# Optimization experiments

Hardware: AMD Instinct MI355X
Metric: run time of the kernel (lower is better)

The kernel has to match this reference:

```python
import jax, jax.numpy as jnp
import numpy as np

B, L, E, D, H, P, NL = 4, 2048, 7, 512, 8, 720, 2
DH = D // H
FACTOR = 5
U = min(L, FACTOR * int(np.ceil(np.log(L))))  # top-u queries, = 40
SCALE = 1.0 / np.sqrt(DH)


def setup_inputs() -> dict:
    key = jax.random.key(0)
    ks = jax.random.split(key, 12)
    s = 0.02
    rn = lambda k, shape: jax.random.normal(k, shape, jnp.float32) * s
    return {
        "x": jax.random.normal(ks[0], (B, L, E), jnp.float32),
        "emb_w": rn(ks[1], (E, D)), "emb_b": jnp.zeros((D,), jnp.float32),
        "Wq": rn(ks[2], (NL, D, D)), "bq": jnp.zeros((NL, D), jnp.float32),
        "Wk": rn(ks[3], (NL, D, D)), "bk": jnp.zeros((NL, D), jnp.float32),
        "Wv": rn(ks[4], (NL, D, D)), "bv": jnp.zeros((NL, D), jnp.float32),
        "Wo": rn(ks[5], (NL, D, D)), "bo": jnp.zeros((NL, D), jnp.float32),
        "W1": rn(ks[6], (NL, D, D)), "b1": jnp.zeros((NL, D), jnp.float32),
        "W2": rn(ks[7], (NL, D, D)), "b2": jnp.zeros((NL, D), jnp.float32),
        "ln1_g": jnp.ones((NL, D), jnp.float32), "ln1_b": jnp.zeros((NL, D), jnp.float32),
        "ln2_g": jnp.ones((NL, D), jnp.float32), "ln2_b": jnp.zeros((NL, D), jnp.float32),
        "proj_w": rn(ks[8], (D, E)), "proj_b": jnp.zeros((E,), jnp.float32),
    }


def layer_norm(x, g, b):
    m = jnp.mean(x, axis=-1, keepdims=True)
    v = jnp.mean(jnp.square(x - m), axis=-1, keepdims=True)
    return (x - m) * jax.lax.rsqrt(v + 1e-5) * g + b


def prob_sparse_attn(x, Wq, bq, Wk, bk, Wv, bv, Wo, bo):
    # x: [B, L, D] -> heads [B, H, L, DH]
    q = (x @ Wq + bq).reshape(B, L, H, DH).transpose(0, 2, 1, 3)
    k = (x @ Wk + bk).reshape(B, L, H, DH).transpose(0, 2, 1, 3)
    v = (x @ Wv + bv).reshape(B, L, H, DH).transpose(0, 2, 1, 3)
    scores = jnp.einsum('bhqd,bhkd->bhqk', q, k) * SCALE  # [B,H,L,L]
    # sparsity measure M(q) = max_k - mean_k
    M = jnp.max(scores, axis=-1) - jnp.mean(scores, axis=-1)  # [B,H,L]
    _, idx = jax.lax.top_k(M, U)  # [B,H,U] indices of active queries
    s_top = jnp.take_along_axis(scores, idx[..., None], axis=2)  # [B,H,U,L]
    attn = jax.nn.softmax(s_top, axis=-1)
    upd = jnp.einsum('bhul,bhld->bhud', attn, v)  # [B,H,U,DH]
    # lazy queries get the mean of V; active queries get attention output
    ctx = jnp.broadcast_to(jnp.mean(v, axis=2, keepdims=True), v.shape)
    bidx = jnp.arange(B)[:, None, None]
    hidx = jnp.arange(H)[None, :, None]
    ctx = ctx.at[bidx, hidx, idx].set(upd)  # scatter active queries
    out = ctx.transpose(0, 2, 1, 3).reshape(B, L, D)
    return out @ Wo + bo


def reference(x, emb_w, emb_b, Wq, bq, Wk, bk, Wv, bv, Wo, bo,
              W1, b1, W2, b2, ln1_g, ln1_b, ln2_g, ln2_b, proj_w, proj_b):
    h = x @ emb_w + emb_b  # [B,L,D]
    for i in range(NL):
        a = prob_sparse_attn(h, Wq[i], bq[i], Wk[i], bk[i], Wv[i], bv[i], Wo[i], bo[i])
        h = layer_norm(h + a, ln1_g[i], ln1_b[i])
        f = jax.nn.relu(h @ W1[i] + b1[i]) @ W2[i] + b2[i]
        h = layer_norm(h + f, ln2_g[i], ln2_b[i])
    return h[:, -P:, :] @ proj_w + proj_b  # [B,P,E]
```

## Files before the change

kernel.cpp:

```cpp
#include <hip/hip_runtime.h>
#include <hip/hip_bf16.h>
#include <cstdint>
#include <cstddef>

#define BB 4
#define LL 2048
#define EE 7
#define DD 512
#define HH 8
#define DHH 64
#define PP 720
#define NLAYER 2
#define UU 40
#define SCALE 0.125f
#define ROWS (BB*LL)
#define BIGN ((size_t)ROWS*DD)
#define NIN 21
#define FCH 256
#define NCH (LL/FCH)
#define PSTR 264
#define VSTR 136

typedef unsigned short u16;
typedef unsigned long long u64;
typedef __bf16 bf16x8 __attribute__((ext_vector_type(8)));
typedef float  f32x4  __attribute__((ext_vector_type(4)));

__device__ __forceinline__ float bf2f(u16 u){
  union { uint32_t i; float f; } c; c.i = ((uint32_t)u) << 16; return c.f;
}
__device__ __forceinline__ u16 f2b(float f){
  __hip_bfloat16 h = __float2bfloat16(f);
  return *(u16*)&h;
}
__device__ __forceinline__ void gld_lds16(const u16* g, u16* l){
  __builtin_amdgcn_global_load_lds(
      (const __attribute__((address_space(1))) uint32_t*)g,
      (__attribute__((address_space(3))) uint32_t*)l, 16, 0, 0);
}
__device__ __forceinline__ int is_bf16(const void* d15){
  return (*(const uint32_t*)d15 == 0x3F800000u) ? 0 : 1;
}

#define NSMALL 15
struct ConvArgs { const void* src[NSMALL]; int off[NSMALL]; int n[NSMALL]; };
struct WPtrs { const void* p[6]; };

__global__ __launch_bounds__(256) void k_preamble(ConvArgs a, WPtrs wp,
    const void* __restrict__ xraw, const void* __restrict__ d15,
    float* __restrict__ dst, float* __restrict__ zbuf,
    u16* __restrict__ hB, u16* __restrict__ wT){
  int y = blockIdx.y, bx = blockIdx.x, t = threadIdx.x;
  int isbf = is_bf16(d15);
  __shared__ u16 tile[64][65];
  __shared__ float xs[32][EE];
  if (y < NSMALL){
    int i = bx*256 + t;
    if (i >= a.n[y]) return;
    float v;
    if (isbf) v = bf2f(((const u16*)a.src[y])[i]);
    else      v = ((const float*)a.src[y])[i];
    dst[(size_t)a.off[y] + i] = v;
  } else if (y == NSMALL){
    int i = bx*256 + t;
    if (i < NLAYER*4096) zbuf[i] = 0.f;
  } else if (y < 32){
    int flat = (y - 16)*256 + bx;
    if (flat >= 512) return;
    int colgrp = flat & 1;
    int rowbase = (flat >> 1) * 32;
    int dd = colgrp*256 + t;
    if (t < 32*EE){
      int j = t / EE, e = t - j*EE;
      xs[j][e] = isbf ? bf2f(((const u16*)xraw)[(rowbase + j)*EE + e])
                      : ((const float*)xraw)[(rowbase + j)*EE + e];
    }
    float wreg[EE];
    #pragma unroll
    for (int e=0;e<EE;e++)
      wreg[e] = isbf ? bf2f(((const u16*)a.src[1])[e*DD + dd])
                     : ((const float*)a.src[1])[e*DD + dd];
    float bias = isbf ? bf2f(((const u16*)a.src[2])[dd]) : ((const float*)a.src[2])[dd];
    __syncthreads();
    for (int j=0;j<32;j++){
      float acc = bias;
      #pragma unroll
      for (int e=0;e<EE;e++) acc = fmaf(xs[j][e], wreg[e], acc);
      hB[(size_t)(rowbase + j)*DD + dd] = f2b(acc);
    }
  } else {
    int flat = (y - 32)*256 + bx;
    int mz = flat >> 6, tl = flat & 63;
    int lay = mz / 6, mat = mz % 6;
    int n0 = (tl & 7)*64, k0 = (tl >> 3)*64;
    int r = t >> 6, c = t & 63;
    const void* src = wp.p[mat];
    for (int rr = r; rr < 64; rr += 4){
      size_t idx = ((size_t)lay*DD + (k0+rr))*DD + n0 + c;
      u16 v;
      if (isbf) v = ((const u16*)src)[idx];
      else      v = f2b(((const float*)src)[idx]);
      tile[rr][c] = v;
    }
    __syncthreads();
    u16* drow = wT + ((size_t)mz*DD + n0)*DD + k0;
    int c4 = (t & 15)*4;
    for (int rr = (t >> 4); rr < 64; rr += 16){
      ushort4 v = { tile[c4][rr], tile[c4+1][rr], tile[c4+2][rr], tile[c4+3][rr] };
      *(ushort4*)(drow + (size_t)rr*DD + c4) = v;
    }
  }
}

__global__ __launch_bounds__(256) void k_gemm_mfma(const u16* __restrict__ A, const u16* __restrict__ Bt,
    const float* __restrict__ bias, u16* __restrict__ Cb, int relu){
  __shared__ u16 As[64*64];
  __shared__ u16 Bs[128*64];
  int t = threadIdx.x, wave = t >> 6, lane = t & 63;
  int qlane = lane & 15, quad = lane >> 4;
  int flat = blockIdx.x + gridDim.x*blockIdx.y;
  int xcd = flat & 7, rest = flat >> 3;
  int mb = (xcd + 8*(rest & 15)) * 64;
  int nb = (rest >> 4) * 128;
  int wm = (wave & 1) * 32, wn = (wave >> 1) * 64;
  f32x4 acc[2][4];
  #pragma unroll
  for (int i=0;i<2;i++)
    #pragma unroll
    for (int j=0;j<4;j++) acc[i][j] = (f32x4){0.f,0.f,0.f,0.f};

  int srow = wave*8 + (lane>>3);
  int scol = (((lane&7) ^ ((lane>>3)&7))) * 8;
  const u16* Ag = A + (size_t)(mb + srow)*DD + scol;
  const u16* Bg = Bt + (size_t)(nb + srow)*DD + scol;

  for (int k0 = 0; k0 < DD; k0 += 64){
    __syncthreads();
    #pragma unroll
    for (int i=0;i<2;i++)
      gld_lds16(Ag + (size_t)i*32*DD + k0, As + (i*32 + wave*8)*64);
    #pragma unroll
    for (int i=0;i<4;i++)
      gld_lds16(Bg + (size_t)i*32*DD + k0, Bs + (i*32 + wave*8)*64);
    __syncthreads();
    #pragma unroll
    for (int ch=0; ch<2; ++ch){
      bf16x8 af[2], bfv[4];
      int cgL = ((ch*4 + quad) ^ (qlane & 7)) * 8;
      #pragma unroll
      for (int i=0;i<2;i++) af[i] = *(const bf16x8*)(As + (wm + i*16 + qlane)*64 + cgL);
      #pragma unroll
      for (int j=0;j<4;j++) bfv[j] = *(const bf16x8*)(Bs + (wn + j*16 + qlane)*64 + cgL);
      #pragma unroll
      for (int i=0;i<2;i++)
        #pragma unroll
        for (int j=0;j<4;j++)
          acc[i][j] = __builtin_amdgcn_mfma_f32_16x16x32_bf16(af[i], bfv[j], acc[i][j], 0, 0, 0);
    }
  }
  #pragma unroll
  for (int i=0;i<2;i++){
    int rbase = mb + wm + i*16 + quad*4;
    #pragma unroll
    for (int j=0;j<4;j++){
      int col = nb + wn + j*16 + qlane;
      float bv = bias[col];
      #pragma unroll
      for (int r=0;r<4;r++){
        float cv = acc[i][j][r] + bv;
        if (relu) cv = fmaxf(cv, 0.f);
        Cb[(size_t)(rbase + r)*DD + col] = f2b(cv);
      }
    }
  }
}

__global__ __launch_bounds__(256) void k_gemm_wo(const u64* __restrict__ rowPtr, const u16* __restrict__ Bt,
    const float* __restrict__ bias, u16* __restrict__ Cb){
  __shared__ u16 As[64*64];
  __shared__ u16 Bs[128*64];
  int t = threadIdx.x, wave = t >> 6, lane = t & 63;
  int qlane = lane & 15, quad = lane >> 4;
  int flat = blockIdx.x + gridDim.x*blockIdx.y;
  int xcd = flat & 7, rest = flat >> 3;
  int mb = (xcd + 8*(rest & 15)) * 64;
  int nb = (rest >> 4) * 128;
  int wm = (wave & 1) * 32, wn = (wave >> 1) * 64;
  f32x4 acc[2][4];
  #pragma unroll
  for (int i=0;i<2;i++)
    #pragma unroll
    for (int j=0;j<4;j++) acc[i][j] = (f32x4){0.f,0.f,0.f,0.f};

  int srow = wave*8 + (lane>>3);
  int scol = (((lane&7) ^ ((lane>>3)&7))) * 8;
  const u16* Bg = Bt + (size_t)(nb + srow)*DD + scol;

  for (int k0 = 0; k0 < DD; k0 += 64){
    int slice = k0 >> 6;
    __syncthreads();
    #pragma unroll
    for (int i=0;i<2;i++){
      int arow = mb + i*32 + srow;
      const u16* src = (const u16*)(uintptr_t)rowPtr[(size_t)arow*8 + slice] + scol;
      gld_lds16(src, As + (i*32 + wave*8)*64);
    }
    #pragma unroll
    for (int i=0;i<4;i++)
      gld_lds16(Bg + (size_t)i*32*DD + k0, Bs + (i*32 + wave*8)*64);
    __syncthreads();
    #pragma unroll
    for (int ch=0; ch<2; ++ch){
      bf16x8 af[2], bfv[4];
      int cgL = ((ch*4 + quad) ^ (qlane & 7)) * 8;
      #pragma unroll
      for (int i=0;i<2;i++) af[i] = *(const bf16x8*)(As + (wm + i*16 + qlane)*64 + cgL);
      #pragma unroll
      for (int j=0;j<4;j++) bfv[j] = *(const bf16x8*)(Bs + (wn + j*16 + qlane)*64 + cgL);
      #pragma unroll
      for (int i=0;i<2;i++)
        #pragma unroll
        for (int j=0;j<4;j++)
          acc[i][j] = __builtin_amdgcn_mfma_f32_16x16x32_bf16(af[i], bfv[j], acc[i][j], 0, 0, 0);
    }
  }
  #pragma unroll
  for (int i=0;i<2;i++){
    int rbase = mb + wm + i*16 + quad*4;
    #pragma unroll
    for (int j=0;j<4;j++){
      int col = nb + wn + j*16 + qlane;
      float bv = bias[col];
      #pragma unroll
      for (int r=0;r<4;r++){
        float cv = acc[i][j][r] + bv;
        Cb[(size_t)(rbase + r)*DD + col] = f2b(cv);
      }
    }
  }
}

__global__ __launch_bounds__(256) void k_gemm_qkv(const u16* __restrict__ A, const u16* __restrict__ Wt,
    const float* __restrict__ bq, const float* __restrict__ bk, const float* __restrict__ bv,
    u16* __restrict__ qB, u16* __restrict__ kB, u16* __restrict__ vB,
    float* __restrict__ ksum, float* __restrict__ vsum){
  __shared__ u16 As[128*64];
  __shared__ u16 Bs[128*64];
  int t = threadIdx.x, wave = t >> 6, lane = t & 63;
  int qlane = lane & 15, quad = lane >> 4;
  int flat = blockIdx.x + gridDim.x*blockIdx.y;
  int xcd = flat & 7, rest = flat >> 3;
  int mb  = (xcd + 8*(rest & 7)) * 128;
  int nbg = (rest >> 3) * 128;
  int sel = nbg >> 9;
  int nb  = nbg & 511;
  const float* bias = (sel==0) ? bq : (sel==1) ? bk : bv;
  u16* out = (sel==0) ? qB : (sel==1) ? kB : vB;
  const u16* Bt = Wt + (size_t)sel*DD*DD;
  int wm = (wave & 1) * 64, wn = (wave >> 1) * 64;
  f32x4 acc[4][4];
  #pragma unroll
  for (int i=0;i<4;i++)
    #pragma unroll
    for (int j=0;j<4;j++) acc[i][j] = (f32x4){0.f,0.f,0.f,0.f};

  int srow = wave*8 + (lane>>3);
  int scol = (((lane&7) ^ ((lane>>3)&7))) * 8;
  const u16* Ag = A + (size_t)(mb + srow)*DD + scol;
  const u16* Bg = Bt + (size_t)(nb + srow)*DD + scol;

  for (int k0 = 0; k0 < DD; k0 += 64){
    __syncthreads();
    #pragma unroll
    for (int i=0;i<4;i++){
      gld_lds16(Ag + (size_t)i*32*DD + k0, As + (i*32 + wave*8)*64);
      gld_lds16(Bg + (size_t)i*32*DD + k0, Bs + (i*32 + wave*8)*64);
    }
    __syncthreads();
    #pragma unroll
    for (int ch=0; ch<2; ++ch){
      bf16x8 af[4], bf[4];
      int cgL = ((ch*4 + quad) ^ (qlane & 7)) * 8;
      #pragma unroll
      for (int i=0;i<4;i++) af[i] = *(const bf16x8*)(As + (wm + i*16 + qlane)*64 + cgL);
      #pragma unroll
      for (int j=0;j<4;j++) bf[j] = *(const bf16x8*)(Bs + (wn + j*16 + qlane)*64 + cgL);
      #pragma unroll
      for (int i=0;i<4;i++)
        #pragma unroll
        for (int j=0;j<4;j++)
          acc[i][j] = __builtin_amdgcn_mfma_f32_16x16x32_bf16(af[i], bf[j], acc[i][j], 0, 0, 0);
    }
  }
  float csum[4] = {0.f,0.f,0.f,0.f};
  #pragma unroll
  for (int j=0;j<4;j++){
    int col = nb + wn + j*16 + qlane;
    float bvv = bias[col];
    #pragma unroll
    for (int i=0;i<4;i++){
      int rbase = mb + wm + i*16 + quad*4;
      #pragma unroll
      for (int r=0;r<4;r++){
        float cv = acc[i][j][r] + bvv;
        out[(size_t)(rbase + r)*DD + col] = f2b(cv);
        csum[j] += cv;
      }
    }
  }
  if (sel > 0){
    float* dst = (sel==1) ? ksum : vsum;
    int bidx = mb >> 11;
    #pragma unroll
    for (int j=0;j<4;j++){
      float v = csum[j];
      v += __shfl_xor(v, 16);
      v += __shfl_xor(v, 32);
      if ((lane>>4) == 0)
        atomicAdd(dst + bidx*512 + nb + wn + j*16 + lane, v);
    }
  }
}

__global__ __launch_bounds__(256) void k_sparsity_mfma(const u16* __restrict__ qB, const u16* __restrict__ kB,
    const float* __restrict__ ksum, float* __restrict__ Mout){
  int flat = blockIdx.x + gridDim.x*blockIdx.y;
  int xcd = flat & 7, rest = flat >> 3;
  int qc = rest & 15;
  int bh = (rest >> 4)*8 + xcd;
  int b = bh >> 3, hh = bh & 7;
  int q0 = qc * 128;
  int t = threadIdx.x, wave = t >> 6, lane = t & 63;
  const u16* qbase = qB + ((size_t)(b*LL + q0))*DD + hh*DHH;
  const u16* kbase = kB + ((size_t)b*LL)*DD + hh*DHH;
  bf16x8 qa[8][2];
  #pragma unroll
  for (int i=0;i<8;i++)
    #pragma unroll
    for (int c=0;c<2;c++)
      qa[i][c] = *(const bf16x8*)(qbase + (size_t)(i*16 + (lane&15))*DD + c*32 + (lane>>4)*8);
  float rmax[8][4];
  #pragma unroll
  for (int i=0;i<8;i++)
    #pragma unroll
    for (int r=0;r<4;r++) rmax[i][r] = -3.0e38f;
  for (int kt = wave*16; kt < LL; kt += 64){
    bf16x8 kb0 = *(const bf16x8*)(kbase + (size_t)(kt + (lane&15))*DD + (lane>>4)*8);
    bf16x8 kb1 = *(const bf16x8*)(kbase + (size_t)(kt + (lane&15))*DD + 32 + (lane>>4)*8);
    #pragma unroll
    for (int i=0;i<8;i++){
      f32x4 a = (f32x4){0.f,0.f,0.f,0.f};
      a = __builtin_amdgcn_mfma_f32_16x16x32_bf16(qa[i][0], kb0, a, 0, 0, 0);
      a = __builtin_amdgcn_mfma_f32_16x16x32_bf16(qa[i][1], kb1, a, 0, 0, 0);
      #pragma unroll
      for (int r=0;r<4;r++) rmax[i][r] = fmaxf(rmax[i][r], a[r]);
    }
  }
  #pragma unroll
  for (int i=0;i<8;i++)
    #pragma unroll
    for (int r=0;r<4;r++){
      float v = rmax[i][r];
      v = fmaxf(v, __shfl_xor(v, 1));
      v = fmaxf(v, __shfl_xor(v, 2));
      v = fmaxf(v, __shfl_xor(v, 4));
      v = fmaxf(v, __shfl_xor(v, 8));
      rmax[i][r] = v;
    }
  __shared__ float smax[4][128];
  if ((lane & 15) == 0){
    #pragma unroll
    for (int i=0;i<8;i++)
      #pragma unroll
      for (int r=0;r<4;r++)
        smax[wave][i*16 + (lane>>4)*4 + r] = rmax[i][r];
  }
  __syncthreads();
  if (t < 128){
    float mx = fmaxf(fmaxf(smax[0][t], smax[1][t]), fmaxf(smax[2][t], smax[3][t]));
    const u16* qrow = qB + (size_t)(b*LL + q0 + t)*DD + hh*DHH;
    float dot = 0.f;
    #pragma unroll
    for (int dv=0; dv<16; ++dv){
      ushort4 qv = *(const ushort4*)(qrow + dv*4);
      const float* kp = ksum + bh*DHH + dv*4;
      dot += bf2f(qv.x)*kp[0] + bf2f(qv.y)*kp[1]
           + bf2f(qv.z)*kp[2] + bf2f(qv.w)*kp[3];
    }
    Mout[bh*LL + q0 + t] = SCALE * (mx - dot * (1.0f/LL));
  }
}

__global__ __launch_bounds__(256) void k_flash(const u16* __restrict__ qB, const u16* __restrict__ kB,
    const u16* __restrict__ vB, const float* __restrict__ Mv, int* __restrict__ sidx,
    float* __restrict__ pO, float* __restrict__ pM, float* __restrict__ pS){
  int bh = blockIdx.y, c = blockIdx.x;
  int b = bh >> 3, hh = bh & 7;
  int t = threadIdx.x, w = t >> 6, lane = t & 63;
  int qlane = lane & 15, quad = lane >> 4;
  int l0 = c * FCH;
  __shared__ u16 Ps[48*PSTR];
  __shared__ union { uint32_t keys[LL]; u16 vst[64*VSTR]; } uu;
  __shared__ float wred[4][48];
  __shared__ float mrow[48];
  __shared__ int hist[256];
  __shared__ int scr[2];
  __shared__ int tieIdx[64];
  __shared__ int counters[2];
  __shared__ int sidxL[UU], sidxS[UU];

  {
    const float* src = Mv + (size_t)bh*LL;
    #pragma unroll
    for (int j = 0; j < 8; ++j){
      int idx = t + j*256;
      uint32_t u = __float_as_uint(src[idx]);
      uu.keys[idx] = (u & 0x80000000u) ? ~u : (u | 0x80000000u);
    }
    uint32_t prefix = 0, pmask = 0;
    int need = UU;
    #pragma unroll
    for (int pass = 0; pass < 4; ++pass){
      int shift = 24 - pass*8;
      __syncthreads();
      hist[t] = 0;
      __syncthreads();
      #pragma unroll
      for (int j = 0; j < 8; ++j){
        uint32_t k = uu.keys[t + j*256];
        if ((k & pmask) == prefix)
          atomicAdd(&hist[(k >> shift) & 0xFF], 1);
      }
      __syncthreads();
      if (t < 64){
        int ln = t;
        int h0 = hist[ln*4+0], h1 = hist[ln*4+1], h2 = hist[ln*4+2], h3 = hist[ln*4+3];
        int s = h0 + h1 + h2 + h3;
        int acc = s;
        #pragma unroll
        for (int off = 1; off < 64; off <<= 1){
          int v = __shfl_down(acc, off);
          if (ln + off < 64) acc += v;
        }
        int c3 = acc - s;
        int c2 = c3 + h3;
        int c1 = c2 + h2;
        int c0 = c1 + h1;
        if      (need > c3 && need <= c3 + h3){ scr[0] = ln*4+3; scr[1] = c3; }
        else if (need > c2 && need <= c2 + h2){ scr[0] = ln*4+2; scr[1] = c2; }
        else if (need > c1 && need <= c1 + h1){ scr[0] = ln*4+1; scr[1] = c1; }
        else if (need > c0 && need <= c0 + h0){ scr[0] = ln*4+0; scr[1] = c0; }
      }
      __syncthreads();
      prefix |= ((uint32_t)scr[0]) << shift;
      need -= scr[1];
      pmask |= 0xFFu << shift;
    }
    if (t < 2) counters[t] = 0;
    __syncthreads();
    uint32_t Tkey = prefix;
    #pragma unroll
    for (int j = 0; j < 8; ++j){
      int idx = t + j*256;
      uint32_t k = uu.keys[idx];
      if (k > Tkey){
        int p = atomicAdd(&counters[0], 1);
        sidxL[p] = idx;
      } else if (k == Tkey){
        int p = atomicAdd(&counters[1], 1);
        if (p < 64) tieIdx[p] = idx;
      }
    }
    __syncthreads();
    if (t == 0){
      int c_gt = counters[0];
      int tc = counters[1];
      int needTies = UU - c_gt;
      if (tc <= 64){
        for (int m = 0; m < needTies; ++m){
          int bestv = 0x7FFFFFFF, bestp = -1;
          for (int q = 0; q < tc; ++q)
            if (tieIdx[q] < bestv){ bestv = tieIdx[q]; bestp = q; }
          sidxL[c_gt + m] = bestv;
          tieIdx[bestp] = 0x7FFFFFFF;
        }
      } else {
        int m = 0;
        for (int j = 0; j < LL && m < needTies; ++j)
          if (uu.keys[j] == Tkey){ sidxL[c_gt + m] = j; m++; }
      }
    }
    __syncthreads();
    int vv = 0, rk = 0;
    if (t < UU){
      vv = sidxL[t];
      #pragma unroll 8
      for (int j = 0; j < UU; ++j) rk += (sidxL[j] < vv) ? 1 : 0;
    }
    __syncthreads();
    if (t < UU) sidxS[rk] = vv;
    __syncthreads();
    if (c == 0 && t < UU) sidx[bh*UU + t] = sidxS[t];
  }

  const u16* kbase = kB + (size_t)b*LL*DD + hh*DHH;
  const u16* vbase = vB + (size_t)b*LL*DD + hh*DHH;
  const u16* qbase = qB + (size_t)b*LL*DD + hh*DHH;

  bf16x8 qa[3][2];
  #pragma unroll
  for (int i=0;i<3;i++){
    int u = i*16 + qlane;
    if (u < UU){
      const u16* qr = qbase + (size_t)sidxS[u]*DD + quad*8;
      qa[i][0] = *(const bf16x8*)qr;
      qa[i][1] = *(const bf16x8*)(qr + 32);
    } else {
      bf16x8 z;
      #pragma unroll
      for (int q8=0;q8<8;q8++) z[q8] = (__bf16)0.0f;
      qa[i][0] = z; qa[i][1] = z;
    }
  }
  f32x4 S[3][4];
  #pragma unroll
  for (int j=0;j<4;j++){
    const u16* kr = kbase + (size_t)(l0 + w*64 + j*16 + qlane)*DD + quad*8;
    bf16x8 k0 = *(const bf16x8*)kr;
    bf16x8 k1 = *(const bf16x8*)(kr + 32);
    #pragma unroll
    for (int i=0;i<3;i++){
      f32x4 a = (f32x4){0.f,0.f,0.f,0.f};
      a = __builtin_amdgcn_mfma_f32_16x16x32_bf16(qa[i][0], k0, a, 0, 0, 0);
      a = __builtin_amdgcn_mfma_f32_16x16x32_bf16(qa[i][1], k1, a, 0, 0, 0);
      S[i][j] = a;
    }
  }
  #pragma unroll
  for (int i=0;i<3;i++){
    #pragma unroll
    for (int r=0;r<4;r++){
      float m = -3.0e38f;
      #pragma unroll
      for (int j=0;j<4;j++){ S[i][j][r] *= SCALE; m = fmaxf(m, S[i][j][r]); }
      m = fmaxf(m, __shfl_xor(m, 1));
      m = fmaxf(m, __shfl_xor(m, 2));
      m = fmaxf(m, __shfl_xor(m, 4));
      m = fmaxf(m, __shfl_xor(m, 8));
      if (qlane == 0) wred[w][i*16 + quad*4 + r] = m;
    }
  }
  __syncthreads();
  if (t < 48) mrow[t] = fmaxf(fmaxf(wred[0][t], wred[1][t]), fmaxf(wred[2][t], wred[3][t]));
  __syncthreads();
  #pragma unroll
  for (int i=0;i<3;i++){
    #pragma unroll
    for (int r=0;r<4;r++){
      int row = i*16 + quad*4 + r;
      float m = mrow[row];
      float ls = 0.f;
      #pragma unroll
      for (int j=0;j<4;j++){
        float e = __expf(S[i][j][r] - m);
        ls += e;
        Ps[row*PSTR + w*64 + j*16 + qlane] = f2b(e);
      }
      ls += __shfl_xor(ls, 1);
      ls += __shfl_xor(ls, 2);
      ls += __shfl_xor(ls, 4);
      ls += __shfl_xor(ls, 8);
      if (qlane == 0) wred[w][row] = ls;
    }
  }
  __syncthreads();
  if (t < 48){
    pM[(bh*NCH + c)*48 + t] = mrow[t];
    pS[(bh*NCH + c)*48 + t] = wred[0][t] + wred[1][t] + wred[2][t] + wred[3][t];
  }
  f32x4 O[3];
  #pragma unroll
  for (int i=0;i<3;i++) O[i] = (f32x4){0.f,0.f,0.f,0.f};
  for (int half = 0; half < 2; ++half){
    __syncthreads();
    for (int idx = t; idx < 128*64; idx += 256){
      int rr = idx >> 6, d = idx & 63;
      uu.vst[d*VSTR + rr] = vbase[(size_t)(l0 + half*128 + rr)*DD + d];
    }
    __syncthreads();
    #pragma unroll
    for (int ks = 0; ks < 4; ++ks){
      int kloc = half*128 + ks*32;
      bf16x8 bfv = *(const bf16x8*)(uu.vst + (w*16 + qlane)*VSTR + ks*32 + quad*8);
      #pragma unroll
      for (int i=0;i<3;i++){
        bf16x8 af = *(const bf16x8*)(Ps + (i*16 + qlane)*PSTR + kloc + quad*8);
        O[i] = __builtin_amdgcn_mfma_f32_16x16x32_bf16(af, bfv, O[i], 0, 0, 0);
      }
    }
  }
  size_t ob = (size_t)(bh*NCH + c)*48*64;
  #pragma unroll
  for (int i=0;i<3;i++)
    #pragma unroll
    for (int r=0;r<4;r++)
      pO[ob + (size_t)(i*16 + quad*4 + r)*64 + w*16 + qlane] = O[i][r];
}

__global__ __launch_bounds__(256) void k_flash_red(const float* __restrict__ pO, const float* __restrict__ pM,
    const float* __restrict__ pS, const int* __restrict__ sidx, const float* __restrict__ vsum,
    u16* __restrict__ attnC, u16* __restrict__ vmeanB, u64* __restrict__ rowPtr){
  int bh = blockIdx.x; int b = bh >> 3, hh = bh & 7;
  int t = threadIdx.x;
  if (t < 64) vmeanB[b*512 + hh*64 + t] = f2b(vsum[b*512 + hh*64 + t] * (1.0f/LL));
  u64 vmPtr = (u64)(uintptr_t)(vmeanB + b*512 + hh*64);
  for (int row = t; row < LL; row += 256)
    rowPtr[((size_t)b*LL + row)*8 + hh] = vmPtr;
  __syncthreads();
  if (t < UU)
    rowPtr[((size_t)b*LL + sidx[bh*UU + t])*8 + hh] =
        (u64)(uintptr_t)(attnC + ((size_t)bh*UU + t)*64);
  for (int idx = t; idx < UU*64; idx += 256){
    int u = idx >> 6, n = idx & 63;
    float m = -3.0e38f;
    #pragma unroll
    for (int c=0;c<NCH;c++) m = fmaxf(m, pM[(bh*NCH + c)*48 + u]);
    float s = 0.f, o = 0.f;
    #pragma unroll
    for (int c=0;c<NCH;c++){
      float wgt = __expf(pM[(bh*NCH + c)*48 + u] - m);
      s += wgt * pS[(bh*NCH + c)*48 + u];
      o += wgt * pO[((size_t)(bh*NCH + c)*48 + u)*64 + n];
    }
    attnC[((size_t)bh*UU + u)*64 + n] = f2b(o / s);
  }
}

__global__ __launch_bounds__(256) void k_addln(const u16* __restrict__ a, const u16* __restrict__ r,
    const float* __restrict__ g, const float* __restrict__ bvec, u16* __restrict__ outB){
  int row = blockIdx.x*4 + (threadIdx.x >> 6);
  int lane = threadIdx.x & 63;
  size_t base = (size_t)row * DD + lane*8;
  ushort4 a0 = *(const ushort4*)(a + base);
  ushort4 a1 = *(const ushort4*)(a + base + 4);
  ushort4 r0 = *(const ushort4*)(r + base);
  ushort4 r1 = *(const ushort4*)(r + base + 4);
  float x[8] = {bf2f(a0.x)+bf2f(r0.x), bf2f(a0.y)+bf2f(r0.y),
                bf2f(a0.z)+bf2f(r0.z), bf2f(a0.w)+bf2f(r0.w),
                bf2f(a1.x)+bf2f(r1.x), bf2f(a1.y)+bf2f(r1.y),
                bf2f(a1.z)+bf2f(r1.z), bf2f(a1.w)+bf2f(r1.w)};
  float s = 0.f;
  #pragma unroll
  for (int i=0;i<8;i++) s += x[i];
  #pragma unroll
  for (int off=1; off<64; off<<=1) s += __shfl_xor(s, off);
  float mean = s * (1.0f/DD);
  float vs = 0.f;
  #pragma unroll
  for (int i=0;i<8;i++){ x[i] -= mean; vs += x[i]*x[i]; }
  #pragma unroll
  for (int off=1; off<64; off<<=1) vs += __shfl_xor(vs, off);
  float rs = rsqrtf(vs * (1.0f/DD) + 1e-5f);
  const float* gp = g + lane*8;
  const float* bp = bvec + lane*8;
  u16 ob[8];
  #pragma unroll
  for (int i=0;i<8;i++) ob[i] = f2b(x[i]*rs*gp[i] + bp[i]);
  *(ushort4*)(outB + base)     = (ushort4){ob[0],ob[1],ob[2],ob[3]};
  *(ushort4*)(outB + base + 4) = (ushort4){ob[4],ob[5],ob[6],ob[7]};
}

__global__ __launch_bounds__(256) void k_proj(const u16* __restrict__ hB, const float* __restrict__ pw,
    const float* __restrict__ pb, void* __restrict__ out, const void* __restrict__ d15){
  int rp = blockIdx.x*4 + (threadIdx.x >> 6);
  int lane = threadIdx.x & 63;
  int b = rp / PP, pp = rp - b*PP;
  const u16* hr = hB + (size_t)(b*LL + (LL-PP) + pp) * DD + lane*8;
  ushort4 v0 = *(const ushort4*)hr;
  ushort4 v1 = *(const ushort4*)(hr + 4);
  float x[8] = {bf2f(v0.x), bf2f(v0.y), bf2f(v0.z), bf2f(v0.w),
                bf2f(v1.x), bf2f(v1.y), bf2f(v1.z), bf2f(v1.w)};
  float acc[EE];
  #pragma unroll
  for (int e=0;e<EE;e++) acc[e]=0.f;
  #pragma unroll
  for (int j=0;j<8;j++){
    const float* wrow = pw + (size_t)(lane*8 + j)*EE;
    #pragma unroll
    for (int e=0;e<EE;e++) acc[e] = fmaf(x[j], wrow[e], acc[e]);
  }
  int isbf = is_bf16(d15);
  #pragma unroll
  for (int e=0;e<EE;e++){
    float rr = acc[e];
    #pragma unroll
    for (int off=32; off>0; off>>=1) rr += __shfl_down(rr, off);
    if (lane == 0){
      float val = rr + pb[e];
      if (isbf) ((__hip_bfloat16*)out)[(size_t)rp*EE + e] = __float2bfloat16(val);
      else      ((float*)out)[(size_t)rp*EE + e] = val;
    }
  }
}

extern "C" void kernel_launch(void* const* d_in, const int* in_sizes, int n_in,
                              void* d_out, int out_size, void* d_ws, size_t ws_size,
                              hipStream_t stream){
  float* ws    = (float*)d_ws;
  float* Mv    = ws;
  float* ksumL = Mv + (size_t)BB*HH*LL;
  float* pM    = ksumL + NLAYER*4096;
  float* pS    = pM + 12288;
  float* pO    = pS + 12288;
  int*   sidx  = (int*)(pO + 786432);
  u64*   rowPtr= (u64*)(((uintptr_t)(sidx + 1280) + 15) & ~(uintptr_t)15);
  u16*   attnC = (u16*)(rowPtr + (size_t)ROWS*8);
  u16*   vmeanB= attnC + (size_t)BB*HH*UU*64;
  u16*   hB    = vmeanB + 2048;
  u16*   qB    = hB + BIGN;
  u16*   kB    = qB + BIGN;
  u16*   vB    = kB + BIGN;
  u16*   f1B   = vB + BIGN;
  u16*   tmpB  = f1B + BIGN;
  u16*   wT    = tmpB + BIGN;
  float* conv  = (float*)(((uintptr_t)(wT + (size_t)12*DD*DD) + 15) & ~(uintptr_t)15);

  static const int small_ids[NSMALL] = {0,1,2,4,6,8,10,12,14,15,16,17,18,19,20};
  ConvArgs ca;
  int off_all[NIN];
  int tot = 0;
  for (int i = 0; i < NIN; ++i) off_all[i] = -1;
  for (int s = 0; s < NSMALL; ++s){
    int i = small_ids[s];
    ca.src[s] = d_in[i];
    ca.off[s] = tot;
    ca.n[s]   = in_sizes[i];
    off_all[i] = tot;
    tot += in_sizes[i];
  }
  const float* bq = conv + off_all[4];
  const float* bk = conv + off_all[6];
  const float* bv = conv + off_all[8];
  const float* bo = conv + off_all[10];
  const float* b1 = conv + off_all[12];
  const float* b2 = conv + off_all[14];
  const float* ln1g = conv + off_all[15]; const float* ln1b = conv + off_all[16];
  const float* ln2g = conv + off_all[17]; const float* ln2b = conv + off_all[18];
  const float* pw = conv + off_all[19]; const float* pb = conv + off_all[20];

  WPtrs wp;
  wp.p[0]=d_in[3]; wp.p[1]=d_in[5]; wp.p[2]=d_in[7];
  wp.p[3]=d_in[9]; wp.p[4]=d_in[11]; wp.p[5]=d_in[13];

  k_preamble<<<dim3(256, 35), 256, 0, stream>>>(ca, wp, d_in[0], d_in[15],
                                                conv, ksumL, hB, wT);

  dim3 gg(4, 128);
  dim3 gq(3*DD/128, ROWS/128);

  for (int l = 0; l < NLAYER; ++l){
    const u16* WqkvT = wT + (size_t)(l*6 + 0)*DD*DD;
    const u16* WoT   = wT + (size_t)(l*6 + 3)*DD*DD;
    const u16* W1T   = wT + (size_t)(l*6 + 4)*DD*DD;
    const u16* W2T   = wT + (size_t)(l*6 + 5)*DD*DD;
    float* ksum = ksumL + l*4096;
    float* vsum = ksum + 2048;

    k_gemm_qkv<<<gq, 256, 0, stream>>>(hB, WqkvT, bq + l*DD, bk + l*DD, bv + l*DD,
                                       qB, kB, vB, ksum, vsum);
    k_sparsity_mfma<<<dim3(LL/128, BB*HH), 256, 0, stream>>>(qB, kB, ksum, Mv);
    k_flash<<<dim3(NCH, BB*HH), 256, 0, stream>>>(qB, kB, vB, Mv, sidx, pO, pM, pS);
    k_flash_red<<<BB*HH, 256, 0, stream>>>(pO, pM, pS, sidx, vsum, attnC, vmeanB, rowPtr);
    k_gemm_wo<<<gg, 256, 0, stream>>>(rowPtr, WoT, bo + l*DD, tmpB);
    k_addln<<<ROWS/4, 256, 0, stream>>>(hB, tmpB, ln1g + l*DD, ln1b + l*DD, hB);
    k_gemm_mfma<<<gg, 256, 0, stream>>>(hB, W1T, b1 + l*DD, f1B, 1);
    k_gemm_mfma<<<gg, 256, 0, stream>>>(f1B, W2T, b2 + l*DD, tmpB, 0);
    k_addln<<<ROWS/4, 256, 0, stream>>>(hB, tmpB, ln2g + l*DD, ln2b + l*DD, hB);
  }
  k_proj<<<(BB*PP)/4, 256, 0, stream>>>(hB, pw, pb, d_out, d_in[15]);
}
```

Baseline: 362.3 us.

## Fuse flash reduction and add+layernorm into producer kernels via last-block counters

Removes the separate flash-reduction kernel and both add+LayerNorm kernels per layer. Each producer kernel now bumps an atomic counter, and the last-arriving block for a row tile or head does the follow-up work in place: the split-softmax merge and row-pointer setup in k_flash, and the residual add plus LayerNorm in k_gemm_wo and the W2 GEMM. This cuts kernel launches and the gaps between dependent kernels. The cost is extra fences and atomics, a serialized tail done by the last block, and reliance on counters in the workspace starting at a multiple of the block count.

```diff
diff --git a/kernel.cpp b/kernel.cpp
--- a/kernel.cpp
+++ b/kernel.cpp
@@ -40,6 +40,39 @@
 }
 __device__ __forceinline__ int is_bf16(const void* d15){
   return (*(const uint32_t*)d15 == 0x3F800000u) ? 0 : 1;
+}
+
+__device__ __forceinline__ void addln_row(const u16* a, const u16* r,
+    const float* g, const float* bvec, u16* outB,
+    int row, int lane){
+  size_t base = (size_t)row * DD + lane*8;
+  ushort4 a0 = *(const ushort4*)(a + base);
+  ushort4 a1 = *(const ushort4*)(a + base + 4);
+  ushort4 r0 = *(const ushort4*)(r + base);
+  ushort4 r1 = *(const ushort4*)(r + base + 4);
+  float x[8] = {bf2f(a0.x)+bf2f(r0.x), bf2f(a0.y)+bf2f(r0.y),
+                bf2f(a0.z)+bf2f(r0.z), bf2f(a0.w)+bf2f(r0.w),
+                bf2f(a1.x)+bf2f(r1.x), bf2f(a1.y)+bf2f(r1.y),
+                bf2f(a1.z)+bf2f(r1.z), bf2f(a1.w)+bf2f(r1.w)};
+  float s = 0.f;
+  #pragma unroll
+  for (int i=0;i<8;i++) s += x[i];
+  #pragma unroll
+  for (int off=1; off<64; off<<=1) s += __shfl_xor(s, off);
+  float mean = s * (1.0f/DD);
+  float vs = 0.f;
+  #pragma unroll
+  for (int i=0;i<8;i++){ x[i] -= mean; vs += x[i]*x[i]; }
+  #pragma unroll
+  for (int off=1; off<64; off<<=1) vs += __shfl_xor(vs, off);
+  float rs = rsqrtf(vs * (1.0f/DD) + 1e-5f);
+  const float* gp = g + lane*8;
+  const float* bp = bvec + lane*8;
+  u16 ob[8];
+  #pragma unroll
+  for (int i=0;i<8;i++) ob[i] = f2b(x[i]*rs*gp[i] + bp[i]);
+  *(ushort4*)(outB + base)     = (ushort4){ob[0],ob[1],ob[2],ob[3]};
+  *(ushort4*)(outB + base + 4) = (ushort4){ob[4],ob[5],ob[6],ob[7]};
 }
 
 #define NSMALL 15
@@ -113,7 +146,9 @@
 }
 
 __global__ __launch_bounds__(256) void k_gemm_mfma(const u16* __restrict__ A, const u16* __restrict__ Bt,
-    const float* __restrict__ bias, u16* __restrict__ Cb, int relu){
+    const float* __restrict__ bias, u16* __restrict__ Cb, int relu,
+    const u16* __restrict__ resid, const float* __restrict__ lng,
+    const float* __restrict__ lnbv, int* __restrict__ cnt){
   __shared__ u16 As[64*64];
   __shared__ u16 Bs[128*64];
   int t = threadIdx.x, wave = t >> 6, lane = t & 63;
@@ -173,10 +208,24 @@
       }
     }
   }
+  if (cnt){
+    __syncthreads();
+    __threadfence();
+    __shared__ int lastB;
+    if (t == 0) lastB = ((atomicAdd(cnt + (mb >> 6), 1) & 3) == 3);
+    __syncthreads();
+    if (lastB){
+      __threadfence();
+      for (int rr = t >> 6; rr < 64; rr += 4)
+        addln_row(resid, Cb, lng, lnbv, (u16*)resid, mb + rr, lane);
+    }
+  }
 }
 
 __global__ __launch_bounds__(256) void k_gemm_wo(const u64* __restrict__ rowPtr, const u16* __restrict__ Bt,
-    const float* __restrict__ bias, u16* __restrict__ Cb){
+    const float* __restrict__ bias, u16* __restrict__ Cb,
+    const u16* __restrict__ resid, const float* __restrict__ lng,
+    const float* __restrict__ lnbv, int* __restrict__ cnt){
   __shared__ u16 As[64*64];
   __shared__ u16 Bs[128*64];
   int t = threadIdx.x, wave = t >> 6, lane = t & 63;
@@ -237,6 +286,16 @@
         Cb[(size_t)(rbase + r)*DD + col] = f2b(cv);
       }
     }
+  }
+  __syncthreads();
+  __threadfence();
+  __shared__ int lastB;
+  if (t == 0) lastB = ((atomicAdd(cnt + (mb >> 6), 1) & 3) == 3);
+  __syncthreads();
+  if (lastB){
+    __threadfence();
+    for (int rr = t >> 6; rr < 64; rr += 4)
+      addln_row(resid, Cb, lng, lnbv, (u16*)resid, mb + rr, lane);
   }
 }
 
@@ -392,8 +451,10 @@
 }
 
 __global__ __launch_bounds__(256) void k_flash(const u16* __restrict__ qB, const u16* __restrict__ kB,
-    const u16* __restrict__ vB, const float* __restrict__ Mv, int* __restrict__ sidx,
-    float* __restrict__ pO, float* __restrict__ pM, float* __restrict__ pS){
+    const u16* __restrict__ vB, const float* __restrict__ Mv,
+    float* __restrict__ pO, float* __restrict__ pM, float* __restrict__ pS,
+    const float* __restrict__ vsum, u16* __restrict__ attnC, u16* __restrict__ vmeanB,
+    u64* __restrict__ rowPtr, int* __restrict__ cntF){
   int bh = blockIdx.y, c = blockIdx.x;
   int b = bh >> 3, hh = bh & 7;
   int t = threadIdx.x, w = t >> 6, lane = t & 63;
@@ -500,7 +561,6 @@
     __syncthreads();
     if (t < UU) sidxS[rk] = vv;
     __syncthreads();
-    if (c == 0 && t < UU) sidx[bh*UU + t] = sidxS[t];
   }
 
   const u16* kbase = kB + (size_t)b*LL*DD + hh*DHH;
@@ -605,69 +665,36 @@
     #pragma unroll
     for (int r=0;r<4;r++)
       pO[ob + (size_t)(i*16 + quad*4 + r)*64 + w*16 + qlane] = O[i][r];
-}
-
-__global__ __launch_bounds__(256) void k_flash_red(const float* __restrict__ pO, const float* __restrict__ pM,
-    const float* __restrict__ pS, const int* __restrict__ sidx, const float* __restrict__ vsum,
-    u16* __restrict__ attnC, u16* __restrict__ vmeanB, u64* __restrict__ rowPtr){
-  int bh = blockIdx.x; int b = bh >> 3, hh = bh & 7;
-  int t = threadIdx.x;
+
+  __syncthreads();
+  __threadfence();
+  __shared__ int lastF;
+  if (t == 0) lastF = ((atomicAdd(cntF + bh, 1) & 7) == 7);
+  __syncthreads();
+  if (!lastF) return;
+  __threadfence();
   if (t < 64) vmeanB[b*512 + hh*64 + t] = f2b(vsum[b*512 + hh*64 + t] * (1.0f/LL));
   u64 vmPtr = (u64)(uintptr_t)(vmeanB + b*512 + hh*64);
   for (int row = t; row < LL; row += 256)
     rowPtr[((size_t)b*LL + row)*8 + hh] = vmPtr;
   __syncthreads();
   if (t < UU)
-    rowPtr[((size_t)b*LL + sidx[bh*UU + t])*8 + hh] =
+    rowPtr[((size_t)b*LL + sidxS[t])*8 + hh] =
         (u64)(uintptr_t)(attnC + ((size_t)bh*UU + t)*64);
   for (int idx = t; idx < UU*64; idx += 256){
     int u = idx >> 6, n = idx & 63;
     float m = -3.0e38f;
     #pragma unroll
-    for (int c=0;c<NCH;c++) m = fmaxf(m, pM[(bh*NCH + c)*48 + u]);
+    for (int cc=0;cc<NCH;cc++) m = fmaxf(m, pM[(bh*NCH + cc)*48 + u]);
     float s = 0.f, o = 0.f;
     #pragma unroll
-    for (int c=0;c<NCH;c++){
-      float wgt = __expf(pM[(bh*NCH + c)*48 + u] - m);
-      s += wgt * pS[(bh*NCH + c)*48 + u];
-      o += wgt * pO[((size_t)(bh*NCH + c)*48 + u)*64 + n];
+    for (int cc=0;cc<NCH;cc++){
+      float wgt = __expf(pM[(bh*NCH + cc)*48 + u] - m);
+      s += wgt * pS[(bh*NCH + cc)*48 + u];
+      o += wgt * pO[((size_t)(bh*NCH + cc)*48 + u)*64 + n];
     }
     attnC[((size_t)bh*UU + u)*64 + n] = f2b(o / s);
   }
-}
-
-__global__ __launch_bounds__(256) void k_addln(const u16* __restrict__ a, const u16* __restrict__ r,
-    const float* __restrict__ g, const float* __restrict__ bvec, u16* __restrict__ outB){
-  int row = blockIdx.x*4 + (threadIdx.x >> 6);
-  int lane = threadIdx.x & 63;
-  size_t base = (size_t)row * DD + lane*8;
-  ushort4 a0 = *(const ushort4*)(a + base);
-  ushort4 a1 = *(const ushort4*)(a + base + 4);
-  ushort4 r0 = *(const ushort4*)(r + base);
-  ushort4 r1 = *(const ushort4*)(r + base + 4);
-  float x[8] = {bf2f(a0.x)+bf2f(r0.x), bf2f(a0.y)+bf2f(r0.y),
-                bf2f(a0.z)+bf2f(r0.z), bf2f(a0.w)+bf2f(r0.w),
-                bf2f(a1.x)+bf2f(r1.x), bf2f(a1.y)+bf2f(r1.y),
-                bf2f(a1.z)+bf2f(r1.z), bf2f(a1.w)+bf2f(r1.w)};
-  float s = 0.f;
-  #pragma unroll
-  for (int i=0;i<8;i++) s += x[i];
-  #pragma unroll
-  for (int off=1; off<64; off<<=1) s += __shfl_xor(s, off);
-  float mean = s * (1.0f/DD);
-  float vs = 0.f;
-  #pragma unroll
-  for (int i=0;i<8;i++){ x[i] -= mean; vs += x[i]*x[i]; }
-  #pragma unroll
-  for (int off=1; off<64; off<<=1) vs += __shfl_xor(vs, off);
-  float rs = rsqrtf(vs * (1.0f/DD) + 1e-5f);
-  const float* gp = g + lane*8;
-  const float* bp = bvec + lane*8;
-  u16 ob[8];
-  #pragma unroll
-  for (int i=0;i<8;i++) ob[i] = f2b(x[i]*rs*gp[i] + bp[i]);
-  *(ushort4*)(outB + base)     = (ushort4){ob[0],ob[1],ob[2],ob[3]};
-  *(ushort4*)(outB + base + 4) = (ushort4){ob[4],ob[5],ob[6],ob[7]};
 }
 
 __global__ __launch_bounds__(256) void k_proj(const u16* __restrict__ hB, const float* __restrict__ pw,
@@ -709,11 +736,13 @@
   float* ws    = (float*)d_ws;
   float* Mv    = ws;
   float* ksumL = Mv + (size_t)BB*HH*LL;
-  float* pM    = ksumL + NLAYER*4096;
+  int*   cntWo = (int*)(ksumL + NLAYER*4096);
+  int*   cntW2 = cntWo + NLAYER*128;
+  int*   cntFl = cntW2 + NLAYER*128;
+  float* pM    = ksumL + NLAYER*4096 + 1024;
   float* pS    = pM + 12288;
   float* pO    = pS + 12288;
-  int*   sidx  = (int*)(pO + 786432);
-  u64*   rowPtr= (u64*)(((uintptr_t)(sidx + 1280) + 15) & ~(uintptr_t)15);
+  u64*   rowPtr= (u64*)(((uintptr_t)(pO + 786432) + 15) & ~(uintptr_t)15);
   u16*   attnC = (u16*)(rowPtr + (size_t)ROWS*8);
   u16*   vmeanB= attnC + (size_t)BB*HH*UU*64;
   u16*   hB    = vmeanB + 2048;
@@ -769,13 +798,15 @@
     k_gemm_qkv<<<gq, 256, 0, stream>>>(hB, WqkvT, bq + l*DD, bk + l*DD, bv + l*DD,
                                        qB, kB, vB, ksum, vsum);
     k_sparsity_mfma<<<dim3(LL/128, BB*HH), 256, 0, stream>>>(qB, kB, ksum, Mv);
-    k_flash<<<dim3(NCH, BB*HH), 256, 0, stream>>>(qB, kB, vB, Mv, sidx, pO, pM, pS);
-    k_flash_red<<<BB*HH, 256, 0, stream>>>(pO, pM, pS, sidx, vsum, attnC, vmeanB, rowPtr);
-    k_gemm_wo<<<gg, 256, 0, stream>>>(rowPtr, WoT, bo + l*DD, tmpB);
-    k_addln<<<ROWS/4, 256, 0, stream>>>(hB, tmpB, ln1g + l*DD, ln1b + l*DD, hB);
-    k_gemm_mfma<<<gg, 256, 0, stream>>>(hB, W1T, b1 + l*DD, f1B, 1);
-    k_gemm_mfma<<<gg, 256, 0, stream>>>(f1B, W2T, b2 + l*DD, tmpB, 0);
-    k_addln<<<ROWS/4, 256, 0, stream>>>(hB, tmpB, ln2g + l*DD, ln2b + l*DD, hB);
+    k_flash<<<dim3(NCH, BB*HH), 256, 0, stream>>>(qB, kB, vB, Mv, pO, pM, pS,
+                                                  vsum, attnC, vmeanB, rowPtr,
+                                                  cntFl + l*32);
+    k_gemm_wo<<<gg, 256, 0, stream>>>(rowPtr, WoT, bo + l*DD, tmpB,
+                                      hB, ln1g + l*DD, ln1b + l*DD, cntWo + l*128);
+    k_gemm_mfma<<<gg, 256, 0, stream>>>(hB, W1T, b1 + l*DD, f1B, 1,
+                                        nullptr, nullptr, nullptr, nullptr);
+    k_gemm_mfma<<<gg, 256, 0, stream>>>(f1B, W2T, b2 + l*DD, tmpB, 0,
+                                        hB, ln2g + l*DD, ln2b + l*DD, cntW2 + l*128);
   }
   k_proj<<<(BB*PP)/4, 256, 0, stream>>>(hB, pw, pb, d_out, d_in[15]);
 }
```

New measurement: 677.4 us. 1.87x slower.

## Fuse post-attention add+LayerNorm into W1 GEMM and final LN into projection

Applied to the files above, without the earlier changes.

The first residual add+LayerNorm is computed inside the W1 GEMM prologue. Each block normalizes its 64 rows into a full-K LDS tile, and the nb==0 blocks also write the normalized rows out as the next residual, using ping-pong h buffers. In the last layer the second add+LayerNorm is folded into the projection kernel, so it only runs on the needed P rows. This removes two LN kernel launches and their global round-trips. In exchange, the LN work is repeated across the 4 column blocks and the kernel needs a 64KB LDS A tile, which may lower occupancy.

```diff
diff --git a/kernel.cpp b/kernel.cpp
--- a/kernel.cpp
+++ b/kernel.cpp
@@ -40,6 +40,35 @@
 }
 __device__ __forceinline__ int is_bf16(const void* d15){
   return (*(const uint32_t*)d15 == 0x3F800000u) ? 0 : 1;
+}
+
+__device__ __forceinline__ void addln_row_vals(const u16* a, const u16* r,
+    const float* g, const float* bvec, int row, int lane, u16 ob[8]){
+  size_t base = (size_t)row * DD + lane*8;
+  ushort4 a0 = *(const ushort4*)(a + base);
+  ushort4 a1 = *(const ushort4*)(a + base + 4);
+  ushort4 r0 = *(const ushort4*)(r + base);
+  ushort4 r1 = *(const ushort4*)(r + base + 4);
+  float x[8] = {bf2f(a0.x)+bf2f(r0.x), bf2f(a0.y)+bf2f(r0.y),
+                bf2f(a0.z)+bf2f(r0.z), bf2f(a0.w)+bf2f(r0.w),
+                bf2f(a1.x)+bf2f(r1.x), bf2f(a1.y)+bf2f(r1.y),
+                bf2f(a1.z)+bf2f(r1.z), bf2f(a1.w)+bf2f(r1.w)};
+  float s = 0.f;
+  #pragma unroll
+  for (int i=0;i<8;i++) s += x[i];
+  #pragma unroll
+  for (int off=1; off<64; off<<=1) s += __shfl_xor(s, off);
+  float mean = s * (1.0f/DD);
+  float vs = 0.f;
+  #pragma unroll
+  for (int i=0;i<8;i++){ x[i] -= mean; vs += x[i]*x[i]; }
+  #pragma unroll
+  for (int off=1; off<64; off<<=1) vs += __shfl_xor(vs, off);
+  float rs = rsqrtf(vs * (1.0f/DD) + 1e-5f);
+  const float* gp = g + lane*8;
+  const float* bp = bvec + lane*8;
+  #pragma unroll
+  for (int i=0;i<8;i++) ob[i] = f2b(x[i]*rs*gp[i] + bp[i]);
 }
 
 #define NSMALL 15
@@ -175,6 +204,83 @@
   }
 }
 
+__global__ __launch_bounds__(256) void k_gemm_w1ln(const u16* __restrict__ hIn, const u16* __restrict__ res,
+    const float* __restrict__ lng, const float* __restrict__ lnbv,
+    const u16* __restrict__ Bt, const float* __restrict__ bias,
+    u16* __restrict__ Cb, u16* __restrict__ hOut){
+  __shared__ u16 AsF[64*512];
+  __shared__ u16 Bs[128*64];
+  int t = threadIdx.x, wave = t >> 6, lane = t & 63;
+  int qlane = lane & 15, quad = lane >> 4;
+  int flat = blockIdx.x + gridDim.x*blockIdx.y;
+  int xcd = flat & 7, rest = flat >> 3;
+  int mb = (xcd + 8*(rest & 15)) * 64;
+  int nb = (rest >> 4) * 128;
+
+  for (int rr = 0; rr < 16; ++rr){
+    int rloc = wave*16 + rr;
+    int row = mb + rloc;
+    u16 ob[8];
+    addln_row_vals(hIn, res, lng, lnbv, row, lane, ob);
+    int p = (lane & ~7) | ((lane & 7) ^ (rloc & 7));
+    *(ushort4*)(AsF + rloc*512 + p*8)     = (ushort4){ob[0],ob[1],ob[2],ob[3]};
+    *(ushort4*)(AsF + rloc*512 + p*8 + 4) = (ushort4){ob[4],ob[5],ob[6],ob[7]};
+    if (nb == 0){
+      size_t base = (size_t)row * DD + lane*8;
+      *(ushort4*)(hOut + base)     = (ushort4){ob[0],ob[1],ob[2],ob[3]};
+      *(ushort4*)(hOut + base + 4) = (ushort4){ob[4],ob[5],ob[6],ob[7]};
+    }
+  }
+
+  int wm = (wave & 1) * 32, wn = (wave >> 1) * 64;
+  f32x4 acc[2][4];
+  #pragma unroll
+  for (int i=0;i<2;i++)
+    #pragma unroll
+    for (int j=0;j<4;j++) acc[i][j] = (f32x4){0.f,0.f,0.f,0.f};
+
+  int srow = wave*8 + (lane>>3);
+  int scol = (((lane&7) ^ ((lane>>3)&7))) * 8;
+  const u16* Bg = Bt + (size_t)(nb + srow)*DD + scol;
+
+  for (int k0 = 0; k0 < DD; k0 += 64){
+    __syncthreads();
+    #pragma unroll
+    for (int i=0;i<4;i++)
+      gld_lds16(Bg + (size_t)i*32*DD + k0, Bs + (i*32 + wave*8)*64);
+    __syncthreads();
+    #pragma unroll
+    for (int ch=0; ch<2; ++ch){
+      bf16x8 af[2], bfv[4];
+      int cgL = ((ch*4 + quad) ^ (qlane & 7)) * 8;
+      int pp = (k0 >> 3) + ((ch*4 + quad) ^ (qlane & 7));
+      #pragma unroll
+      for (int i=0;i<2;i++) af[i] = *(const bf16x8*)(AsF + (wm + i*16 + qlane)*512 + pp*8);
+      #pragma unroll
+      for (int j=0;j<4;j++) bfv[j] = *(const bf16x8*)(Bs + (wn + j*16 + qlane)*64 + cgL);
+      #pragma unroll
+      for (int i=0;i<2;i++)
+        #pragma unroll
+        for (int j=0;j<4;j++)
+          acc[i][j] = __builtin_amdgcn_mfma_f32_16x16x32_bf16(af[i], bfv[j], acc[i][j], 0, 0, 0);
+    }
+  }
+  #pragma unroll
+  for (int i=0;i<2;i++){
+    int rbase = mb + wm + i*16 + quad*4;
+    #pragma unroll
+    for (int j=0;j<4;j++){
+      int col = nb + wn + j*16 + qlane;
+      float bv = bias[col];
+      #pragma unroll
+      for (int r=0;r<4;r++){
+        float cv = fmaxf(acc[i][j][r] + bv, 0.f);
+        Cb[(size_t)(rbase + r)*DD + col] = f2b(cv);
+      }
+    }
+  }
+}
+
 __global__ __launch_bounds__(256) void k_gemm_wo(const u64* __restrict__ rowPtr, const u16* __restrict__ Bt,
     const float* __restrict__ bias, u16* __restrict__ Cb){
   __shared__ u16 As[64*64];
@@ -640,46 +746,26 @@
     const float* __restrict__ g, const float* __restrict__ bvec, u16* __restrict__ outB){
   int row = blockIdx.x*4 + (threadIdx.x >> 6);
   int lane = threadIdx.x & 63;
+  u16 ob[8];
+  addln_row_vals(a, r, g, bvec, row, lane, ob);
   size_t base = (size_t)row * DD + lane*8;
-  ushort4 a0 = *(const ushort4*)(a + base);
-  ushort4 a1 = *(const ushort4*)(a + base + 4);
-  ushort4 r0 = *(const ushort4*)(r + base);
-  ushort4 r1 = *(const ushort4*)(r + base + 4);
-  float x[8] = {bf2f(a0.x)+bf2f(r0.x), bf2f(a0.y)+bf2f(r0.y),
-                bf2f(a0.z)+bf2f(r0.z), bf2f(a0.w)+bf2f(r0.w),
-                bf2f(a1.x)+bf2f(r1.x), bf2f(a1.y)+bf2f(r1.y),
-                bf2f(a1.z)+bf2f(r1.z), bf2f(a1.w)+bf2f(r1.w)};
-  float s = 0.f;
-  #pragma unroll
-  for (int i=0;i<8;i++) s += x[i];
-  #pragma unroll
-  for (int off=1; off<64; off<<=1) s += __shfl_xor(s, off);
-  float mean = s * (1.0f/DD);
-  float vs = 0.f;
-  #pragma unroll
-  for (int i=0;i<8;i++){ x[i] -= mean; vs += x[i]*x[i]; }
-  #pragma unroll
-  for (int off=1; off<64; off<<=1) vs += __shfl_xor(vs, off);
-  float rs = rsqrtf(vs * (1.0f/DD) + 1e-5f);
-  const float* gp = g + lane*8;
-  const float* bp = bvec + lane*8;
-  u16 ob[8];
-  #pragma unroll
-  for (int i=0;i<8;i++) ob[i] = f2b(x[i]*rs*gp[i] + bp[i]);
   *(ushort4*)(outB + base)     = (ushort4){ob[0],ob[1],ob[2],ob[3]};
   *(ushort4*)(outB + base + 4) = (ushort4){ob[4],ob[5],ob[6],ob[7]};
 }
 
-__global__ __launch_bounds__(256) void k_proj(const u16* __restrict__ hB, const float* __restrict__ pw,
-    const float* __restrict__ pb, void* __restrict__ out, const void* __restrict__ d15){
-  int rp = blockIdx.x*4 + (threadIdx.x >> 6);
-  int lane = threadIdx.x & 63;
+__global__ __launch_bounds__(256) void k_proj_ln(const u16* __restrict__ hIn, const u16* __restrict__ res,
+    const float* __restrict__ lng, const float* __restrict__ lnbv,
+    const float* __restrict__ pw, const float* __restrict__ pb,
+    void* __restrict__ out, const void* __restrict__ d15){
+  int w = threadIdx.x >> 6, lane = threadIdx.x & 63;
+  int rp = blockIdx.x*4 + w;
   int b = rp / PP, pp = rp - b*PP;
-  const u16* hr = hB + (size_t)(b*LL + (LL-PP) + pp) * DD + lane*8;
-  ushort4 v0 = *(const ushort4*)hr;
-  ushort4 v1 = *(const ushort4*)(hr + 4);
-  float x[8] = {bf2f(v0.x), bf2f(v0.y), bf2f(v0.z), bf2f(v0.w),
-                bf2f(v1.x), bf2f(v1.y), bf2f(v1.z), bf2f(v1.w)};
+  int row = b*LL + (LL-PP) + pp;
+  u16 ob[8];
+  addln_row_vals(hIn, res, lng, lnbv, row, lane, ob);
+  float x[8];
+  #pragma unroll
+  for (int j=0;j<8;j++) x[j] = bf2f(ob[j]);
   float acc[EE];
   #pragma unroll
   for (int e=0;e<EE;e++) acc[e]=0.f;
@@ -716,13 +802,14 @@
   u64*   rowPtr= (u64*)(((uintptr_t)(sidx + 1280) + 15) & ~(uintptr_t)15);
   u16*   attnC = (u16*)(rowPtr + (size_t)ROWS*8);
   u16*   vmeanB= attnC + (size_t)BB*HH*UU*64;
-  u16*   hB    = vmeanB + 2048;
-  u16*   qB    = hB + BIGN;
+  u16*   h0    = vmeanB + 2048;
+  u16*   qB    = h0 + BIGN;
   u16*   kB    = qB + BIGN;
   u16*   vB    = kB + BIGN;
   u16*   f1B   = vB + BIGN;
   u16*   tmpB  = f1B + BIGN;
-  u16*   wT    = tmpB + BIGN;
+  u16*   h1    = tmpB + BIGN;
+  u16*   wT    = h1 + BIGN;
   float* conv  = (float*)(((uintptr_t)(wT + (size_t)12*DD*DD) + 15) & ~(uintptr_t)15);
 
   static const int small_ids[NSMALL] = {0,1,2,4,6,8,10,12,14,15,16,17,18,19,20};
@@ -753,11 +840,13 @@
   wp.p[3]=d_in[9]; wp.p[4]=d_in[11]; wp.p[5]=d_in[13];
 
   k_preamble<<<dim3(256, 35), 256, 0, stream>>>(ca, wp, d_in[0], d_in[15],
-                                                conv, ksumL, hB, wT);
+                                                conv, ksumL, h0, wT);
 
   dim3 gg(4, 128);
   dim3 gq(3*DD/128, ROWS/128);
 
+  u16* hP[2] = { h0, h1 };
+  int cur = 0;
   for (int l = 0; l < NLAYER; ++l){
     const u16* WqkvT = wT + (size_t)(l*6 + 0)*DD*DD;
     const u16* WoT   = wT + (size_t)(l*6 + 3)*DD*DD;
@@ -765,17 +854,24 @@
     const u16* W2T   = wT + (size_t)(l*6 + 5)*DD*DD;
     float* ksum = ksumL + l*4096;
     float* vsum = ksum + 2048;
-
-    k_gemm_qkv<<<gq, 256, 0, stream>>>(hB, WqkvT, bq + l*DD, bk + l*DD, bv + l*DD,
+    u16* hC = hP[cur];
+    u16* hN = hP[cur ^ 1];
+
+    k_gemm_qkv<<<gq, 256, 0, stream>>>(hC, WqkvT, bq + l*DD, bk + l*DD, bv + l*DD,
                                        qB, kB, vB, ksum, vsum);
     k_sparsity_mfma<<<dim3(LL/128, BB*HH), 256, 0, stream>>>(qB, kB, ksum, Mv);
     k_flash<<<dim3(NCH, BB*HH), 256, 0, stream>>>(qB, kB, vB, Mv, sidx, pO, pM, pS);
     k_flash_red<<<BB*HH, 256, 0, stream>>>(pO, pM, pS, sidx, vsum, attnC, vmeanB, rowPtr);
     k_gemm_wo<<<gg, 256, 0, stream>>>(rowPtr, WoT, bo + l*DD, tmpB);
-    k_addln<<<ROWS/4, 256, 0, stream>>>(hB, tmpB, ln1g + l*DD, ln1b + l*DD, hB);
-    k_gemm_mfma<<<gg, 256, 0, stream>>>(hB, W1T, b1 + l*DD, f1B, 1);
+    k_gemm_w1ln<<<gg, 256, 0, stream>>>(hC, tmpB, ln1g + l*DD, ln1b + l*DD,
+                                        W1T, b1 + l*DD, f1B, hN);
     k_gemm_mfma<<<gg, 256, 0, stream>>>(f1B, W2T, b2 + l*DD, tmpB, 0);
-    k_addln<<<ROWS/4, 256, 0, stream>>>(hB, tmpB, ln2g + l*DD, ln2b + l*DD, hB);
-  }
-  k_proj<<<(BB*PP)/4, 256, 0, stream>>>(hB, pw, pb, d_out, d_in[15]);
-}
+    if (l < NLAYER - 1){
+      k_addln<<<ROWS/4, 256, 0, stream>>>(hN, tmpB, ln2g + l*DD, ln2b + l*DD, hN);
+      cur ^= 1;
+    } else {
+      k_proj_ln<<<(BB*PP)/4, 256, 0, stream>>>(hN, tmpB, ln2g + l*DD, ln2b + l*DD,
+                                               pw, pb, d_out, d_in[15]);
+    }
+  }
+}
```

New measurement: 373.9 us. 1.03x slower.
